# Performance work log

Measured on AMD Instinct MI355X. Metric: run time of the kernel, lower is better.

Reference implementation:

```python
import jax, jax.numpy as jnp
import numpy as np

N = 100000
E = 1600000
NFEAT = 128
NHID = 128
NCLASS = 10


def setup_inputs() -> dict:
    key = jax.random.key(0)
    ks = jax.random.split(key, 12)
    x = jax.random.normal(ks[0], (N, NFEAT), dtype=jnp.float32)
    edge_index = jax.random.randint(ks[1], (2, E), 0, N, dtype=jnp.int64)
    s = 0.05
    W1 = jax.random.normal(ks[2], (NFEAT, NHID), dtype=jnp.float32) * s
    b1 = jnp.zeros((NHID,), dtype=jnp.float32)
    W2 = jax.random.normal(ks[3], (NHID, NHID), dtype=jnp.float32) * s
    b2 = jnp.zeros((NHID,), dtype=jnp.float32)
    W3 = jax.random.normal(ks[4], (NHID, NHID), dtype=jnp.float32) * s
    b3 = jnp.zeros((NHID,), dtype=jnp.float32)
    Wl = jax.random.normal(ks[5], (NHID, NCLASS), dtype=jnp.float32) * s
    bl = jnp.zeros((NCLASS,), dtype=jnp.float32)
    return {"x": x, "edge_index": edge_index, "W1": W1, "b1": b1,
            "W2": W2, "b2": b2, "W3": W3, "b3": b3, "Wl": Wl, "bl": bl}


def _gcn_norm(edge_index, num_nodes):
    # PyG gcn_norm with add_self_loops=True and unit edge weights.
    loops = jnp.arange(num_nodes, dtype=edge_index.dtype)
    src = jnp.concatenate([edge_index[0], loops])  # [E+N]
    dst = jnp.concatenate([edge_index[1], loops])
    ones = jnp.ones(src.shape[0], dtype=jnp.float32)
    deg = jax.ops.segment_sum(ones, dst, num_segments=num_nodes)
    dis = jax.lax.rsqrt(deg)  # deg >= 1 due to self-loops
    norm = dis[src] * dis[dst]  # [E+N]
    return src, dst, norm


def _gcn_conv(h, src, dst, norm, W, b, num_nodes):
    h = h @ W                                   # [N, out]
    msg = h[src] * norm[:, None]                # gather + edge scaling
    out = jax.ops.segment_sum(msg, dst, num_segments=num_nodes)
    return out + b


def reference(x, edge_index, W1, b1, W2, b2, W3, b3, Wl, bl):
    src, dst, norm = _gcn_norm(edge_index, N)
    h = jax.nn.relu(_gcn_conv(x, src, dst, norm, W1, b1, N))
    h = jax.nn.relu(_gcn_conv(h, src, dst, norm, W2, b2, N))
    h = _gcn_conv(h, src, dst, norm, W3, b3, N)
    logits = h @ Wl + bl                        # dropout is identity (eval / p=0)
    return jax.nn.log_softmax(logits, axis=1)
```

## Files before the change

### kernel.cpp

```cpp
#include <hip/hip_runtime.h>

#define NFEAT 128
#define NCLS  10
#define NCP   16
#define BROW  512
#define BINC  4096

static inline size_t alignup(size_t x) { return (x + 255) & ~size_t(255); }

__device__ __forceinline__ ushort f2bf(float f) {
  uint x = __float_as_uint(f);
  return (ushort)((x + 0x7fffu + ((x >> 16) & 1u)) >> 16);
}
__device__ __forceinline__ float bf2f(ushort u) {
  return __uint_as_float(((uint)u) << 16);
}

typedef short bf16x8 __attribute__((ext_vector_type(8)));
typedef float f32x4 __attribute__((ext_vector_type(4)));


__global__ void zero_ints(int* __restrict__ p, int n) {
  int i = blockIdx.x * 256 + threadIdx.x;
  if (i < n) p[i] = 0;
}

__global__ __launch_bounds__(256) void bucket_hist(const int* __restrict__ dst,
                                                   int* __restrict__ bkt_cnt,
                                                   int e, int nbkt) {
  __shared__ int hist[256];
  for (int t = threadIdx.x; t < nbkt; t += 256) hist[t] = 0;
  __syncthreads();
  int i = blockIdx.x * 256 + threadIdx.x;
  int stride = gridDim.x * 256;
  for (; i < e; i += stride) atomicAdd(&hist[dst[i] >> 9], 1);
  __syncthreads();
  for (int t = threadIdx.x; t < nbkt; t += 256)
    if (hist[t]) atomicAdd(&bkt_cnt[t], hist[t]);
}

__global__ __launch_bounds__(256) void bkt_scan(const int* __restrict__ bkt_cnt,
                                                int* __restrict__ bkt_off,
                                                int* __restrict__ gfrontier,
                                                int n, int nbkt) {
  __shared__ int sbuf[256];
  const int t = threadIdx.x;
  int x = 0;
  if (t < nbkt) {
    int lo = t << 9;
    int nodes = n - lo; if (nodes > BROW) nodes = BROW;
    x = bkt_cnt[t] + nodes;
  }
  sbuf[t] = x;
  __syncthreads();
  for (int off = 1; off < 256; off <<= 1) {
    int v = (t >= off) ? sbuf[t - off] : 0;
    __syncthreads();
    sbuf[t] += v;
    __syncthreads();
  }
  if (t < nbkt) { bkt_off[t] = sbuf[t] - x; gfrontier[t] = sbuf[t] - x; }
  if (t == nbkt - 1) bkt_off[nbkt] = sbuf[t];
}

__global__ __launch_bounds__(256) void bin_items(const int* __restrict__ ei,
                                                 int nE, int total, int nbkt,
                                                 int* __restrict__ gfrontier,
                                                 int2* __restrict__ binned) {
  __shared__ int hist[256];
  __shared__ int loff[256];
  __shared__ int gbase[256];
  __shared__ int sbuf[256];
  __shared__ int2 st[BINC];
  const int t = threadIdx.x;
  const int chunk0 = blockIdx.x * BINC;
  for (int q = t; q < nbkt; q += 256) hist[q] = 0;
  __syncthreads();
  for (int j = t; j < BINC; j += 256) {
    int i = chunk0 + j;
    if (i < total) {
      int d = (i < nE) ? ei[nE + i] : (i - nE);
      atomicAdd(&hist[d >> 9], 1);
    }
  }
  __syncthreads();
  int x = (t < nbkt) ? hist[t] : 0;
  sbuf[t] = x;
  __syncthreads();
  for (int off = 1; off < 256; off <<= 1) {
    int v = (t >= off) ? sbuf[t - off] : 0;
    __syncthreads();
    sbuf[t] += v;
    __syncthreads();
  }
  loff[t] = sbuf[t] - x;
  gbase[t] = (t < nbkt && x > 0) ? atomicAdd(&gfrontier[t], x) : 0;
  __syncthreads();
  hist[t] = loff[t];
  __syncthreads();
  for (int j = t; j < BINC; j += 256) {
    int i = chunk0 + j;
    if (i < total) {
      int s, d;
      if (i < nE) { s = ei[i]; d = ei[nE + i]; }
      else        { s = i - nE; d = s; }
      int p = atomicAdd(&hist[d >> 9], 1);
      st[p] = make_int2(s, d);
    }
  }
  __syncthreads();
  int M = total - chunk0; if (M > BINC) M = BINC;
  for (int j = t; j < M; j += 256) {
    int2 it = st[j];
    int b = it.y >> 9;
    binned[gbase[b] + (j - loff[b])] = it;
  }
}

__global__ __launch_bounds__(512) void bucket_finalize(const int2* __restrict__ binned,
                                                       const int* __restrict__ bkt_off,
                                                       int* __restrict__ row_ptr,
                                                       float* __restrict__ dis,
                                                       int* __restrict__ ev,
                                                       int n, int nbkt) {
  __shared__ int hist[BROW];
  __shared__ int sbuf[BROW];
  __shared__ int pre[BROW];
  __shared__ int front[BROW];
  const int b = blockIdx.x;
  const int t = threadIdx.x;
  const int row0 = b << 9;
  const int beg = bkt_off[b], end = bkt_off[b + 1];
  hist[t] = 0; front[t] = 0;
  __syncthreads();
  for (int j = beg + t; j < end; j += BROW)
    atomicAdd(&hist[binned[j].y - row0], 1);
  __syncthreads();
  const int x = hist[t];
  const int v = row0 + t;
  if (v < n) dis[v] = rsqrtf((float)x);
  sbuf[t] = x;
  __syncthreads();
  for (int off = 1; off < BROW; off <<= 1) {
    int val = (t >= off) ? sbuf[t - off] : 0;
    __syncthreads();
    sbuf[t] += val;
    __syncthreads();
  }
  pre[t] = sbuf[t] - x;
  if (v < n) row_ptr[v] = beg + pre[t];
  if (b == nbkt - 1 && t == 0) row_ptr[n] = end;
  __syncthreads();
  for (int j = beg + t; j < end; j += BROW) {
    int2 it = binned[j];
    int dl = it.y - row0;
    int slot = atomicAdd(&front[dl], 1);
    ev[beg + pre[dl] + slot] = it.x;
  }
}


__global__ __launch_bounds__(256) void fold_weights(const float* __restrict__ W3,
                                                    const float* __restrict__ Wl,
                                                    const float* __restrict__ b3,
                                                    const float* __restrict__ bl,
                                                    float* __restrict__ Wf,
                                                    float* __restrict__ bf) {
  int t = blockIdx.x * blockDim.x + threadIdx.x;
  if (t < NFEAT * NCP) {
    int r = t >> 4, c = t & 15;
    float s = 0.f;
    if (c < NCLS) {
      for (int k = 0; k < NFEAT; ++k) s += W3[r * NFEAT + k] * Wl[k * NCLS + c];
    }
    Wf[t] = s;
  }
  if (t < NCP) {
    float s = 0.f;
    if (t < NCLS) {
      s = bl[t];
      for (int k = 0; k < NFEAT; ++k) s += b3[k] * Wl[k * NCLS + t];
    }
    bf[t] = s;
  }
}

__global__ __launch_bounds__(256) void prep_w(const float* __restrict__ W,
                                              ushort* __restrict__ Wt) {
  int t = blockIdx.x * 256 + threadIdx.x;
  if (t < NFEAT * NFEAT) {
    int n = t >> 7, k = t & 127;
    Wt[n * NFEAT + k] = f2bf(W[k * NFEAT + n]);
  }
}


template<bool BF16IN>
__global__ __launch_bounds__(256) void gemm_mfma(const float* __restrict__ A,
                                                 const ushort* __restrict__ Ab,
                                                 const ushort* __restrict__ Wt,
                                                 const float* __restrict__ dis,
                                                 ushort* __restrict__ Cb, int nrows) {
  __shared__ __align__(16) ushort Asm[64 * NFEAT];
  const int tid = threadIdx.x;
  const int row0 = blockIdx.x * 64;
  {
    const int m = tid >> 2;
    const int kc = (tid & 3) * 32;
    const int gr = row0 + m;
    int4 u[4];
    if (BF16IN) {
      if (gr < nrows) {
        const ushort* p = Ab + (size_t)gr * NFEAT + kc;
        u[0] = *(const int4*)(p + 0);
        u[1] = *(const int4*)(p + 8);
        u[2] = *(const int4*)(p + 16);
        u[3] = *(const int4*)(p + 24);
      } else {
        u[0] = u[1] = u[2] = u[3] = make_int4(0, 0, 0, 0);
      }
    } else {
      float4 f[8];
      if (gr < nrows) {
        #pragma unroll
        for (int q = 0; q < 8; ++q)
          f[q] = *(const float4*)&A[(size_t)gr * NFEAT + kc + q * 4];
      } else {
        #pragma unroll
        for (int q = 0; q < 8; ++q) f[q] = make_float4(0.f, 0.f, 0.f, 0.f);
      }
      #pragma unroll
      for (int q = 0; q < 4; ++q) {
        union { ushort us[8]; int4 v; } pk;
        const float* fp = (const float*)&f[q * 2];
        #pragma unroll
        for (int j = 0; j < 8; ++j) pk.us[j] = f2bf(fp[j]);
        u[q] = pk.v;
      }
    }
    #pragma unroll
    for (int q = 0; q < 4; ++q) {
      int byte = (m * 256 + (kc + q * 8) * 2) ^ ((m & 7) << 4);
      *(int4*)((char*)Asm + byte) = u[q];
    }
  }
  __syncthreads();
  const int wave = tid >> 6;
  const int lane = tid & 63;
  const int m0 = wave * 16;
  bf16x8 afr[4];
  #pragma unroll
  for (int ks = 0; ks < 4; ++ks) {
    int m = m0 + (lane & 15);
    int kk = ks * 32 + (lane >> 4) * 8;
    int byte = (m * 256 + kk * 2) ^ ((m & 7) << 4);
    afr[ks] = *(const bf16x8*)((const char*)Asm + byte);
  }
  f32x4 acc[8];
  #pragma unroll
  for (int c = 0; c < 8; ++c) acc[c] = (f32x4){0.f, 0.f, 0.f, 0.f};
  #pragma unroll
  for (int c = 0; c < 8; ++c) {
    #pragma unroll
    for (int ks = 0; ks < 4; ++ks) {
      int n = c * 16 + (lane & 15);
      int kk = ks * 32 + (lane >> 4) * 8;
      bf16x8 bfr = *(const bf16x8*)&Wt[n * NFEAT + kk];
      acc[c] = __builtin_amdgcn_mfma_f32_16x16x32_bf16(afr[ks], bfr, acc[c], 0, 0, 0);
    }
  }
  const int gr_base = row0 + m0 + (lane >> 4) * 4;
  float dr[4];
  #pragma unroll
  for (int r = 0; r < 4; ++r)
    dr[r] = (gr_base + r < nrows) ? dis[gr_base + r] : 0.f;
  #pragma unroll
  for (int c = 0; c < 8; ++c) {
    #pragma unroll
    for (int r = 0; r < 4; ++r) {
      int gr = gr_base + r;
      if (gr < nrows)
        Cb[(size_t)gr * NFEAT + c * 16 + (lane & 15)] = f2bf(acc[c][r] * dr[r]);
    }
  }
}


__global__ __launch_bounds__(256) void aggregate(const ushort* __restrict__ hw,
                                                 const int* __restrict__ row_ptr,
                                                 const int* __restrict__ ev,
                                                 const float* __restrict__ dis,
                                                 const float* __restrict__ bias,
                                                 ushort* __restrict__ outb,
                                                 int relu, int n) {
  const int wave = threadIdx.x >> 6;
  const int lane = threadIdx.x & 63;
  const int v = blockIdx.x * 4 + wave;
  if (v >= n) return;
  const int beg = row_ptr[v], end = row_ptr[v + 1];
  const int half = lane >> 5;
  const int hl = lane & 31;
  float4 acc = make_float4(0.f, 0.f, 0.f, 0.f);
  int e = beg + half;
  for (; e + 6 < end; e += 8) {
    int s0 = ev[e];
    int s1 = ev[e + 2];
    int s2 = ev[e + 4];
    int s3 = ev[e + 6];
    ushort4 q0 = *(const ushort4*)&hw[(size_t)s0 * NFEAT + hl * 4];
    ushort4 q1 = *(const ushort4*)&hw[(size_t)s1 * NFEAT + hl * 4];
    ushort4 q2 = *(const ushort4*)&hw[(size_t)s2 * NFEAT + hl * 4];
    ushort4 q3 = *(const ushort4*)&hw[(size_t)s3 * NFEAT + hl * 4];
    acc.x += bf2f(q0.x) + bf2f(q1.x) + bf2f(q2.x) + bf2f(q3.x);
    acc.y += bf2f(q0.y) + bf2f(q1.y) + bf2f(q2.y) + bf2f(q3.y);
    acc.z += bf2f(q0.z) + bf2f(q1.z) + bf2f(q2.z) + bf2f(q3.z);
    acc.w += bf2f(q0.w) + bf2f(q1.w) + bf2f(q2.w) + bf2f(q3.w);
  }
  for (; e < end; e += 2) {
    int s = ev[e];
    ushort4 q = *(const ushort4*)&hw[(size_t)s * NFEAT + hl * 4];
    acc.x += bf2f(q.x); acc.y += bf2f(q.y);
    acc.z += bf2f(q.z); acc.w += bf2f(q.w);
  }
  acc.x += __shfl_xor(acc.x, 32);
  acc.y += __shfl_xor(acc.y, 32);
  acc.z += __shfl_xor(acc.z, 32);
  acc.w += __shfl_xor(acc.w, 32);
  if (half == 0) {
    float dv = dis[v];
    float4 b = *(const float4*)&bias[hl * 4];
    acc.x = fmaf(acc.x, dv, b.x); acc.y = fmaf(acc.y, dv, b.y);
    acc.z = fmaf(acc.z, dv, b.z); acc.w = fmaf(acc.w, dv, b.w);
    if (relu) {
      acc.x = fmaxf(acc.x, 0.f); acc.y = fmaxf(acc.y, 0.f);
      acc.z = fmaxf(acc.z, 0.f); acc.w = fmaxf(acc.w, 0.f);
    }
    union { ushort us[4]; uint2 q2; } pk;
    pk.us[0] = f2bf(acc.x); pk.us[1] = f2bf(acc.y);
    pk.us[2] = f2bf(acc.z); pk.us[3] = f2bf(acc.w);
    *(uint2*)&outb[(size_t)v * NFEAT + hl * 4] = pk.q2;
  }
}


__global__ __launch_bounds__(256) void gemm_small(const ushort* __restrict__ Ab,
                                                  const float* __restrict__ Wf,
                                                  const float* __restrict__ dis,
                                                  float* __restrict__ G, int n) {
  __shared__ float Ws[NFEAT * NCP];
  for (int i = threadIdx.x; i < NFEAT * NCP; i += 256) Ws[i] = Wf[i];
  __syncthreads();
  const int v = blockIdx.x * 256 + threadIdx.x;
  if (v >= n) return;
  float acc[NCP];
  #pragma unroll
  for (int c = 0; c < NCP; ++c) acc[c] = 0.f;
  #pragma unroll
  for (int p = 0; p < 8; ++p) {
    union { ushort us[16]; int4 q[2]; } a;
    const ushort* pl = Ab + (size_t)v * NFEAT + p * 16;
    a.q[0] = *(const int4*)pl;
    a.q[1] = *(const int4*)(pl + 8);
    #pragma unroll
    for (int j = 0; j < 16; ++j) {
      float av = bf2f(a.us[j]);
      int k = p * 16 + j;
      #pragma unroll
      for (int cq = 0; cq < NCP; cq += 4) {
        float4 w = *(const float4*)&Ws[k * NCP + cq];
        acc[cq + 0] += av * w.x;
        acc[cq + 1] += av * w.y;
        acc[cq + 2] += av * w.z;
        acc[cq + 3] += av * w.w;
      }
    }
  }
  const float dv = dis[v];
  #pragma unroll
  for (int cq = 0; cq < NCP; cq += 4)
    *(float4*)&G[(size_t)v * NCP + cq] =
        make_float4(acc[cq] * dv, acc[cq + 1] * dv, acc[cq + 2] * dv, acc[cq + 3] * dv);
}


__global__ __launch_bounds__(256) void agg_logits(const float* __restrict__ G,
                                                  const int* __restrict__ row_ptr,
                                                  const int* __restrict__ ev,
                                                  const float* __restrict__ dis,
                                                  const float* __restrict__ bf,
                                                  float* __restrict__ out, int n) {
  const int wave = threadIdx.x >> 6;
  const int lane = threadIdx.x & 63;
  const int v = blockIdx.x * 4 + wave;
  if (v >= n) return;
  const int beg = row_ptr[v], end = row_ptr[v + 1];
  const int g = lane >> 4;
  const int f = lane & 15;
  float acc = 0.f;
  int e = beg + g;
  for (; e + 4 < end; e += 8) {
    int s0 = ev[e];
    int s1 = ev[e + 4];
    acc += G[(size_t)s0 * NCP + f] + G[(size_t)s1 * NCP + f];
  }
  for (; e < end; e += 4) {
    acc += G[(size_t)ev[e] * NCP + f];
  }
  acc += __shfl_xor(acc, 16);
  acc += __shfl_xor(acc, 32);
  float logit = dis[v] * acc + bf[f];
  float pv = (f < NCLS) ? logit : -INFINITY;
  float m = pv;
  #pragma unroll
  for (int s = 8; s >= 1; s >>= 1) m = fmaxf(m, __shfl_xor(m, s));
  float ex = (f < NCLS) ? expf(logit - m) : 0.f;
  float ssum = ex;
  #pragma unroll
  for (int s = 8; s >= 1; s >>= 1) ssum += __shfl_xor(ssum, s);
  float lse = m + logf(ssum);
  if (g == 0 && f < NCLS) out[(size_t)v * NCLS + f] = logit - lse;
}


extern "C" void kernel_launch(void* const* d_in, const int* in_sizes, int n_in,
                              void* d_out, int out_size, void* d_ws, size_t ws_size,
                              hipStream_t stream) {
  const float* x  = (const float*)d_in[0];
  const int*   ei = (const int*)d_in[1];
  const float* W1 = (const float*)d_in[2];
  const float* b1 = (const float*)d_in[3];
  const float* W2 = (const float*)d_in[4];
  const float* b2 = (const float*)d_in[5];
  const float* W3 = (const float*)d_in[6];
  const float* b3 = (const float*)d_in[7];
  const float* Wl = (const float*)d_in[8];
  const float* bl = (const float*)d_in[9];
  float* out = (float*)d_out;

  const int nN = in_sizes[0] / NFEAT;
  const int nE = in_sizes[1] / 2;
  const int total = nN + nE;
  const int nbkt = (nN + BROW - 1) >> 9;
  const int nbBin = (total + BINC - 1) / BINC;

  char* ws = (char*)d_ws;
  int*    bkt_cnt = (int*)ws;     ws += alignup(256 * 4);
  int*    bkt_off = (int*)ws;     ws += alignup(257 * 4);
  int*    gfront  = (int*)ws;     ws += alignup(256 * 4);
  int*    row_ptr = (int*)ws;     ws += alignup((size_t)(nN + 1) * 4);
  float*  dis     = (float*)ws;   ws += alignup((size_t)nN * 4);
  float*  Wf      = (float*)ws;   ws += alignup((size_t)NFEAT * NCP * 4);
  float*  bfv     = (float*)ws;   ws += alignup((size_t)NCP * 4);
  ushort* Wt1     = (ushort*)ws;  ws += alignup((size_t)NFEAT * NFEAT * 2);
  ushort* Wt2     = (ushort*)ws;  ws += alignup((size_t)NFEAT * NFEAT * 2);
  int2*   binned  = (int2*)ws;    ws += alignup((size_t)total * 8);
  int*    ev      = (int*)ws;     ws += alignup((size_t)total * 4);
  ushort* hb      = (ushort*)ws;  ws += alignup((size_t)nN * NFEAT * 2);
  ushort* hbA     = (ushort*)ws;  ws += alignup((size_t)nN * NFEAT * 2);
  float*  G       = (float*)ws;   ws += alignup((size_t)nN * NCP * 4);

  zero_ints<<<1, 256, 0, stream>>>(bkt_cnt, nbkt);
  bucket_hist<<<512, 256, 0, stream>>>(ei + nE, bkt_cnt, nE, nbkt);
  bkt_scan<<<1, 256, 0, stream>>>(bkt_cnt, bkt_off, gfront, nN, nbkt);
  bin_items<<<nbBin, 256, 0, stream>>>(ei, nE, total, nbkt, gfront, binned);
  bucket_finalize<<<nbkt, BROW, 0, stream>>>(binned, bkt_off, row_ptr, dis, ev, nN, nbkt);

  fold_weights<<<8, 256, 0, stream>>>(W3, Wl, b3, bl, Wf, bfv);
  prep_w<<<64, 256, 0, stream>>>(W1, Wt1);
  prep_w<<<64, 256, 0, stream>>>(W2, Wt2);

  const int gemm_grid = (nN + 63) / 64;
  const int node_grid = (nN + 3) / 4;

  gemm_mfma<false><<<gemm_grid, 256, 0, stream>>>(x, nullptr, Wt1, dis, hb, nN);
  aggregate<<<node_grid, 256, 0, stream>>>(hb, row_ptr, ev, dis, b1, hbA, 1, nN);
  gemm_mfma<true><<<gemm_grid, 256, 0, stream>>>(nullptr, hbA, Wt2, dis, hb, nN);
  aggregate<<<node_grid, 256, 0, stream>>>(hb, row_ptr, ev, dis, b2, hbA, 1, nN);
  gemm_small<<<(nN + 255) / 256, 256, 0, stream>>>(hbA, Wf, dis, G, nN);
  agg_logits<<<node_grid, 256, 0, stream>>>(G, row_ptr, ev, dis, bfv, out, nN);
}
```

Measured before the change: 355.6 us.

## Pack binned edges into 32-bit words, store logit features as bf16, merge prep kernels

Binned edge items now hold the source index and the local destination row in one 32-bit word instead of an int2. This halves the write and read traffic between bin_items and bucket_finalize. The intermediate G matrix from gemm_small is stored as bf16, which halves the gather traffic in agg_logits at some cost in precision. The weight preparation kernels are merged into one launch, and the zeroing kernel is replaced by hipMemsetAsync; packing the source index into 17 bits assumes fewer than 131072 nodes.

```diff
diff --git a/kernel.cpp b/kernel.cpp
--- a/kernel.cpp
+++ b/kernel.cpp
@@ -19,11 +19,6 @@
 typedef short bf16x8 __attribute__((ext_vector_type(8)));
 typedef float f32x4 __attribute__((ext_vector_type(4)));
 
-
-__global__ void zero_ints(int* __restrict__ p, int n) {
-  int i = blockIdx.x * 256 + threadIdx.x;
-  if (i < n) p[i] = 0;
-}
 
 __global__ __launch_bounds__(256) void bucket_hist(const int* __restrict__ dst,
                                                    int* __restrict__ bkt_cnt,
@@ -66,7 +61,7 @@
 __global__ __launch_bounds__(256) void bin_items(const int* __restrict__ ei,
                                                  int nE, int total, int nbkt,
                                                  int* __restrict__ gfrontier,
-                                                 int2* __restrict__ binned) {
+                                                 uint* __restrict__ binned) {
   __shared__ int hist[256];
   __shared__ int loff[256];
   __shared__ int gbase[256];
@@ -113,11 +108,12 @@
   for (int j = t; j < M; j += 256) {
     int2 it = st[j];
     int b = it.y >> 9;
-    binned[gbase[b] + (j - loff[b])] = it;
-  }
-}
-
-__global__ __launch_bounds__(512) void bucket_finalize(const int2* __restrict__ binned,
+    uint pk = (uint)it.x | ((uint)(it.y & 511) << 17);
+    binned[gbase[b] + (j - loff[b])] = pk;
+  }
+}
+
+__global__ __launch_bounds__(512) void bucket_finalize(const uint* __restrict__ binned,
                                                        const int* __restrict__ bkt_off,
                                                        int* __restrict__ row_ptr,
                                                        float* __restrict__ dis,
@@ -134,7 +130,7 @@
   hist[t] = 0; front[t] = 0;
   __syncthreads();
   for (int j = beg + t; j < end; j += BROW)
-    atomicAdd(&hist[binned[j].y - row0], 1);
+    atomicAdd(&hist[binned[j] >> 17], 1);
   __syncthreads();
   const int x = hist[t];
   const int v = row0 + t;
@@ -152,45 +148,47 @@
   if (b == nbkt - 1 && t == 0) row_ptr[n] = end;
   __syncthreads();
   for (int j = beg + t; j < end; j += BROW) {
-    int2 it = binned[j];
-    int dl = it.y - row0;
+    uint pk = binned[j];
+    int dl = pk >> 17;
     int slot = atomicAdd(&front[dl], 1);
-    ev[beg + pre[dl] + slot] = it.x;
-  }
-}
-
-
-__global__ __launch_bounds__(256) void fold_weights(const float* __restrict__ W3,
-                                                    const float* __restrict__ Wl,
-                                                    const float* __restrict__ b3,
-                                                    const float* __restrict__ bl,
-                                                    float* __restrict__ Wf,
-                                                    float* __restrict__ bf) {
-  int t = blockIdx.x * blockDim.x + threadIdx.x;
-  if (t < NFEAT * NCP) {
+    ev[beg + pre[dl] + slot] = (int)(pk & 0x1FFFFu);
+  }
+}
+
+
+__global__ __launch_bounds__(256) void prep_all(const float* __restrict__ W1,
+                                                const float* __restrict__ W2,
+                                                const float* __restrict__ W3,
+                                                const float* __restrict__ Wl,
+                                                const float* __restrict__ b3,
+                                                const float* __restrict__ bl,
+                                                ushort* __restrict__ Wt1,
+                                                ushort* __restrict__ Wt2,
+                                                float* __restrict__ Wf,
+                                                float* __restrict__ bf) {
+  const int bid = blockIdx.x;
+  if (bid < 8) {
+    int t = bid * 256 + threadIdx.x;
     int r = t >> 4, c = t & 15;
     float s = 0.f;
     if (c < NCLS) {
       for (int k = 0; k < NFEAT; ++k) s += W3[r * NFEAT + k] * Wl[k * NCLS + c];
     }
     Wf[t] = s;
-  }
-  if (t < NCP) {
-    float s = 0.f;
-    if (t < NCLS) {
-      s = bl[t];
-      for (int k = 0; k < NFEAT; ++k) s += b3[k] * Wl[k * NCLS + t];
-    }
-    bf[t] = s;
-  }
-}
-
-__global__ __launch_bounds__(256) void prep_w(const float* __restrict__ W,
-                                              ushort* __restrict__ Wt) {
-  int t = blockIdx.x * 256 + threadIdx.x;
-  if (t < NFEAT * NFEAT) {
-    int n = t >> 7, k = t & 127;
-    Wt[n * NFEAT + k] = f2bf(W[k * NFEAT + n]);
+    if (t < NCP) {
+      float sb = 0.f;
+      if (t < NCLS) {
+        sb = bl[t];
+        for (int k = 0; k < NFEAT; ++k) sb += b3[k] * Wl[k * NCLS + t];
+      }
+      bf[t] = sb;
+    }
+  } else {
+    int t = (bid - 8) * 256 + threadIdx.x;
+    int u = t & 16383;
+    int n = u >> 7, k = u & 127;
+    if (t < 16384) Wt1[n * NFEAT + k] = f2bf(W1[k * NFEAT + n]);
+    else           Wt2[n * NFEAT + k] = f2bf(W2[k * NFEAT + n]);
   }
 }
 
@@ -346,7 +344,7 @@
 __global__ __launch_bounds__(256) void gemm_small(const ushort* __restrict__ Ab,
                                                   const float* __restrict__ Wf,
                                                   const float* __restrict__ dis,
-                                                  float* __restrict__ G, int n) {
+                                                  ushort* __restrict__ Gb, int n) {
   __shared__ float Ws[NFEAT * NCP];
   for (int i = threadIdx.x; i < NFEAT * NCP; i += 256) Ws[i] = Wf[i];
   __syncthreads();
@@ -376,14 +374,15 @@
     }
   }
   const float dv = dis[v];
-  #pragma unroll
-  for (int cq = 0; cq < NCP; cq += 4)
-    *(float4*)&G[(size_t)v * NCP + cq] =
-        make_float4(acc[cq] * dv, acc[cq + 1] * dv, acc[cq + 2] * dv, acc[cq + 3] * dv);
-}
-
-
-__global__ __launch_bounds__(256) void agg_logits(const float* __restrict__ G,
+  union { ushort us[16]; int4 q[2]; } pk;
+  #pragma unroll
+  for (int c = 0; c < NCP; ++c) pk.us[c] = f2bf(acc[c] * dv);
+  *(int4*)&Gb[(size_t)v * NCP + 0] = pk.q[0];
+  *(int4*)&Gb[(size_t)v * NCP + 8] = pk.q[1];
+}
+
+
+__global__ __launch_bounds__(256) void agg_logits(const ushort* __restrict__ Gb,
                                                   const int* __restrict__ row_ptr,
                                                   const int* __restrict__ ev,
                                                   const float* __restrict__ dis,
@@ -401,10 +400,10 @@
   for (; e + 4 < end; e += 8) {
     int s0 = ev[e];
     int s1 = ev[e + 4];
-    acc += G[(size_t)s0 * NCP + f] + G[(size_t)s1 * NCP + f];
+    acc += bf2f(Gb[(size_t)s0 * NCP + f]) + bf2f(Gb[(size_t)s1 * NCP + f]);
   }
   for (; e < end; e += 4) {
-    acc += G[(size_t)ev[e] * NCP + f];
+    acc += bf2f(Gb[(size_t)ev[e] * NCP + f]);
   }
   acc += __shfl_xor(acc, 16);
   acc += __shfl_xor(acc, 32);
@@ -453,21 +452,19 @@
   float*  bfv     = (float*)ws;   ws += alignup((size_t)NCP * 4);
   ushort* Wt1     = (ushort*)ws;  ws += alignup((size_t)NFEAT * NFEAT * 2);
   ushort* Wt2     = (ushort*)ws;  ws += alignup((size_t)NFEAT * NFEAT * 2);
-  int2*   binned  = (int2*)ws;    ws += alignup((size_t)total * 8);
+  uint*   binned  = (uint*)ws;    ws += alignup((size_t)total * 4);
   int*    ev      = (int*)ws;     ws += alignup((size_t)total * 4);
   ushort* hb      = (ushort*)ws;  ws += alignup((size_t)nN * NFEAT * 2);
   ushort* hbA     = (ushort*)ws;  ws += alignup((size_t)nN * NFEAT * 2);
-  float*  G       = (float*)ws;   ws += alignup((size_t)nN * NCP * 4);
-
-  zero_ints<<<1, 256, 0, stream>>>(bkt_cnt, nbkt);
+  ushort* Gb      = (ushort*)ws;  ws += alignup((size_t)nN * NCP * 2);
+
+  hipMemsetAsync(bkt_cnt, 0, 256 * sizeof(int), stream);
   bucket_hist<<<512, 256, 0, stream>>>(ei + nE, bkt_cnt, nE, nbkt);
   bkt_scan<<<1, 256, 0, stream>>>(bkt_cnt, bkt_off, gfront, nN, nbkt);
   bin_items<<<nbBin, 256, 0, stream>>>(ei, nE, total, nbkt, gfront, binned);
   bucket_finalize<<<nbkt, BROW, 0, stream>>>(binned, bkt_off, row_ptr, dis, ev, nN, nbkt);
 
-  fold_weights<<<8, 256, 0, stream>>>(W3, Wl, b3, bl, Wf, bfv);
-  prep_w<<<64, 256, 0, stream>>>(W1, Wt1);
-  prep_w<<<64, 256, 0, stream>>>(W2, Wt2);
+  prep_all<<<136, 256, 0, stream>>>(W1, W2, W3, Wl, b3, bl, Wt1, Wt2, Wf, bfv);
 
   const int gemm_grid = (nN + 63) / 64;
   const int node_grid = (nN + 3) / 4;
@@ -476,6 +473,6 @@
   aggregate<<<node_grid, 256, 0, stream>>>(hb, row_ptr, ev, dis, b1, hbA, 1, nN);
   gemm_mfma<true><<<gemm_grid, 256, 0, stream>>>(nullptr, hbA, Wt2, dis, hb, nN);
   aggregate<<<node_grid, 256, 0, stream>>>(hb, row_ptr, ev, dis, b2, hbA, 1, nN);
-  gemm_small<<<(nN + 255) / 256, 256, 0, stream>>>(hbA, Wf, dis, G, nN);
-  agg_logits<<<node_grid, 256, 0, stream>>>(G, row_ptr, ev, dis, bfv, out, nN);
-}
+  gemm_small<<<(nN + 255) / 256, 256, 0, stream>>>(hbA, Wf, dis, Gb, nN);
+  agg_logits<<<node_grid, 256, 0, stream>>>(Gb, row_ptr, ev, dis, bfv, out, nN);
+}
```

Result: no change. 353.2 us (-0.7%).
